# Optimization experiments

Measured on AMD Instinct MI355X. Metric: run time of the kernel, lower is better.

Reference implementation:

```python
import jax, jax.numpy as jnp
import numpy as np

N_NODES = 100000
N_EDGES = 1600000
D_IN = 128
D_HID = 128


def setup_inputs() -> dict:
    key = jax.random.key(0)
    k1, k2, k3, k4 = jax.random.split(key, 4)
    x = jax.random.normal(k1, (N_NODES, D_IN), dtype=jnp.float32)
    edge_index = jax.random.randint(k2, (2, N_EDGES), 0, N_NODES, dtype=jnp.int32)
    # glorot-style init for the two GCNConv linear weights
    s1 = (6.0 / (D_IN + D_HID)) ** 0.5
    s2 = (6.0 / (D_HID + D_HID)) ** 0.5
    W1 = jax.random.uniform(k3, (D_IN, D_HID), dtype=jnp.float32, minval=-s1, maxval=s1)
    W2 = jax.random.uniform(k4, (D_HID, D_HID), dtype=jnp.float32, minval=-s2, maxval=s2)
    b1 = jnp.zeros((D_HID,), dtype=jnp.float32)
    b2 = jnp.zeros((D_HID,), dtype=jnp.float32)
    return {"x": x, "edge_index": edge_index, "W1": W1, "b1": b1, "W2": W2, "b2": b2}


def _gcn_conv(h, src, dst, norm, W, b, num_nodes):
    # PyG GCNConv: linear transform, then normalized scatter-add aggregation, then bias.
    h = h @ W                                   # [N, D]
    msg = h[src] * norm[:, None]                # [E+N, D] gathered + scaled messages
    agg = jax.ops.segment_sum(msg, dst, num_segments=num_nodes)
    return agg + b


def reference(x, edge_index, W1, b1, W2, b2):
    n = x.shape[0]
    loops = jnp.arange(n, dtype=edge_index.dtype)
    src = jnp.concatenate([edge_index[0], loops])  # add self-loops
    dst = jnp.concatenate([edge_index[1], loops])
    # symmetric normalization D^{-1/2} (A+I) D^{-1/2}, degree computed on targets
    deg = jax.ops.segment_sum(jnp.ones_like(dst, dtype=x.dtype), dst, num_segments=n)
    dinv = jnp.where(deg > 0, jax.lax.rsqrt(jnp.maximum(deg, 1.0)), 0.0)
    norm = dinv[src] * dinv[dst]
    h = jax.nn.relu(_gcn_conv(x, src, dst, norm, W1, b1, n))
    h = jax.nn.relu(_gcn_conv(h, src, dst, norm, W2, b2, n))
    return h
```

## Files before the change

### kernel.cpp

```cpp
#include <hip/hip_runtime.h>

#define D 128
#define BSH 8
#define BNODES (1 << BSH)
#define NCHUNK 512
#define MAXB 512

typedef __attribute__((ext_vector_type(8))) __bf16 bf16x8;
typedef __attribute__((ext_vector_type(4))) float f32x4;

__device__ __forceinline__ unsigned short f2bf(float f) {
    unsigned int u = __float_as_uint(f);
    u += 0x7fffu + ((u >> 16) & 1u);
    return (unsigned short)(u >> 16);
}
__device__ __forceinline__ float lo_f(unsigned u) { return __uint_as_float(u << 16); }
__device__ __forceinline__ float hi_f(unsigned u) { return __uint_as_float(u & 0xffff0000u); }


__global__ __launch_bounds__(256) void k_hist(const int* __restrict__ dst,
                                              int* __restrict__ cnts,
                                              int E, int nbkt, int chunk) {
    __shared__ int hist[MAXB];
    int c = blockIdx.x;
    int t = threadIdx.x;
    for (int i = t; i < nbkt; i += 256) hist[i] = 0;
    __syncthreads();
    int e0 = c * chunk, e1 = min(e0 + chunk, E);
    for (int e = e0 + t; e < e1; e += 256) atomicAdd(&hist[dst[e] >> BSH], 1);
    __syncthreads();
    for (int i = t; i < nbkt; i += 256) cnts[(size_t)i * NCHUNK + c] = hist[i];
}

__global__ __launch_bounds__(256) void k_chunksum(int* __restrict__ cnts,
                                                  int* __restrict__ btot, int nbkt) {
    int b = blockIdx.x * 4 + (threadIdx.x >> 6);
    if (b >= nbkt) return;
    int l = threadIdx.x & 63;
    int carry = 0;
    for (int g = 0; g < NCHUNK; g += 64) {
        int v = cnts[(size_t)b * NCHUNK + g + l];
        int x = v;
#pragma unroll
        for (int off = 1; off < 64; off <<= 1) {
            int u = __shfl_up(x, off);
            if (l >= off) x += u;
        }
        cnts[(size_t)b * NCHUNK + g + l] = carry + x - v;
        carry += __shfl(x, 63);
    }
    if (l == 0) btot[b] = carry;
}

__global__ __launch_bounds__(MAXB) void k_bktscan(const int* __restrict__ btot,
                                                  int* __restrict__ bbase, int nbkt) {
    __shared__ int s[MAXB];
    int t = threadIdx.x;
    int v = (t < nbkt) ? btot[t] : 0;
    s[t] = v;
    __syncthreads();
    for (int off = 1; off < MAXB; off <<= 1) {
        int u = (t >= off) ? s[t - off] : 0;
        __syncthreads();
        s[t] += u;
        __syncthreads();
    }
    if (t < nbkt) bbase[t + 1] = s[t];
    if (t == 0) bbase[0] = 0;
}

__global__ __launch_bounds__(256) void k_place(const int* __restrict__ src,
                                               const int* __restrict__ dst,
                                               const int* __restrict__ cnts,
                                               const int* __restrict__ bbase,
                                               unsigned* __restrict__ pairs,
                                               int E, int nbkt, int chunk) {
    __shared__ int cur[MAXB];
    int c = blockIdx.x;
    int t = threadIdx.x;
    for (int i = t; i < nbkt; i += 256)
        cur[i] = bbase[i] + cnts[(size_t)i * NCHUNK + c];
    __syncthreads();
    int e0 = c * chunk, e1 = min(e0 + chunk, E);
    for (int e = e0 + t; e < e1; e += 256) {
        int d = dst[e];
        int p = atomicAdd(&cur[d >> BSH], 1);
        pairs[p] = ((unsigned)(d & (BNODES - 1)) << 24) | (unsigned)src[e];
    }
}

__global__ __launch_bounds__(BNODES) void k_build(const unsigned* __restrict__ pairs,
                                                  const int* __restrict__ bbase,
                                                  int* __restrict__ rp,
                                                  float* __restrict__ dinv,
                                                  int* __restrict__ col, int N) {
    __shared__ int cntL[BNODES];
    __shared__ int lcur[BNODES];
    int b = blockIdx.x;
    int n0 = b << BSH;
    int t = threadIdx.x;
    int e0 = bbase[b], e1 = bbase[b + 1];

    cntL[t] = 0;
    __syncthreads();
    for (int e = e0 + t; e < e1; e += BNODES)
        atomicAdd(&cntL[pairs[e] >> 24], 1);
    __syncthreads();
    int deg = cntL[t];
    for (int off = 1; off < BNODES; off <<= 1) {
        int u = (t >= off) ? cntL[t - off] : 0;
        __syncthreads();
        cntL[t] += u;
        __syncthreads();
    }
    int rpv = e0 + cntL[t] - deg;
    lcur[t] = rpv;
    int node = n0 + t;
    if (node < N) {
        rp[node] = rpv;
        dinv[node] = rsqrtf((float)deg + 1.0f);
        if (node == N - 1) rp[N] = e1;
    }
    __syncthreads();
    for (int e = e0 + t; e < e1; e += BNODES) {
        unsigned v = pairs[e];
        int p = atomicAdd(&lcur[v >> 24], 1);
        col[p] = (int)(v & 0x00FFFFFFu);
    }
}

__global__ __launch_bounds__(256) void k_cvt(const float* __restrict__ x,
                                             const float* __restrict__ dinv,
                                             unsigned short* __restrict__ y, int nchunk) {
    int g = blockIdx.x * blockDim.x + threadIdx.x;
    if (g >= nchunk) return;
    int row = g >> 5;
    float s = dinv[row];
    float4 v = reinterpret_cast<const float4*>(x)[g];
    ushort4 o;
    o.x = f2bf(v.x * s);
    o.y = f2bf(v.y * s);
    o.z = f2bf(v.z * s);
    o.w = f2bf(v.w * s);
    reinterpret_cast<ushort4*>(y)[g] = o;
}

__global__ __launch_bounds__(256) void k_agg(const unsigned short* __restrict__ y,
                                             unsigned* __restrict__ outp,
                                             const int* __restrict__ col,
                                             const int* __restrict__ rp,
                                             const float* __restrict__ dinv, int n) {
    int node = blockIdx.x * 4 + (threadIdx.x >> 6);
    if (node >= n) return;
    int c = threadIdx.x & 63;
    const unsigned* yv = reinterpret_cast<const unsigned*>(y);

    unsigned v = yv[(size_t)node * 64 + c];
    float a0 = lo_f(v), a1 = hi_f(v);

    int e0 = rp[node], e1 = rp[node + 1];
    int e = e0;
    for (; e + 8 <= e1; e += 8) {
        int s[8];
#pragma unroll
        for (int i = 0; i < 8; ++i) s[i] = col[e + i];
        unsigned u[8];
#pragma unroll
        for (int i = 0; i < 8; ++i) u[i] = yv[(size_t)s[i] * 64 + c];
#pragma unroll
        for (int i = 0; i < 8; ++i) { a0 += lo_f(u[i]); a1 += hi_f(u[i]); }
    }
    for (; e + 4 <= e1; e += 4) {
        int s0 = col[e], s1 = col[e + 1], s2 = col[e + 2], s3 = col[e + 3];
        unsigned u0 = yv[(size_t)s0 * 64 + c];
        unsigned u1 = yv[(size_t)s1 * 64 + c];
        unsigned u2 = yv[(size_t)s2 * 64 + c];
        unsigned u3 = yv[(size_t)s3 * 64 + c];
        a0 += (lo_f(u0) + lo_f(u1)) + (lo_f(u2) + lo_f(u3));
        a1 += (hi_f(u0) + hi_f(u1)) + (hi_f(u2) + hi_f(u3));
    }
    for (; e < e1; ++e) {
        unsigned u = yv[(size_t)col[e] * 64 + c];
        a0 += lo_f(u);
        a1 += hi_f(u);
    }
    float dn = dinv[node];
    unsigned o = ((unsigned)f2bf(a1 * dn) << 16) | (unsigned)f2bf(a0 * dn);
    outp[(size_t)node * 64 + c] = o;
}

template <int STORE_BF16>
__global__ __launch_bounds__(256) void k_mfma(const unsigned short* __restrict__ A,
                                              const float* __restrict__ W,
                                              const float* __restrict__ bias,
                                              float* __restrict__ out_f32,
                                              unsigned short* __restrict__ out_bf16,
                                              const float* __restrict__ dinv, int N) {
    __shared__ unsigned short Wt[128][136];
    int tid = threadIdx.x;
#pragma unroll
    for (int i = 0; i < 64; ++i) {
        int idx = tid + i * 256;
        int k = idx >> 7, c = idx & 127;
        Wt[c][k] = f2bf(W[idx]);
    }
    __syncthreads();

    int wv = tid >> 6, l = tid & 63;
    int lr = l & 15, lg = l >> 4;
    int r0 = blockIdx.x * 128 + wv * 32;

    f32x4 acc[2][8];
#pragma unroll
    for (int mi = 0; mi < 2; ++mi)
#pragma unroll
        for (int nf = 0; nf < 8; ++nf) acc[mi][nf] = (f32x4)(0.0f);

#pragma unroll
    for (int k0 = 0; k0 < 128; k0 += 32) {
        bf16x8 a[2];
#pragma unroll
        for (int mi = 0; mi < 2; ++mi) {
            int r = r0 + mi * 16 + lr;
            if (r >= N) r = N - 1;
            a[mi] = *reinterpret_cast<const bf16x8*>(&A[(size_t)r * 128 + k0 + lg * 8]);
        }
#pragma unroll
        for (int nf = 0; nf < 8; ++nf) {
            bf16x8 b = *reinterpret_cast<const bf16x8*>(&Wt[nf * 16 + lr][k0 + lg * 8]);
            acc[0][nf] = __builtin_amdgcn_mfma_f32_16x16x32_bf16(a[0], b, acc[0][nf], 0, 0, 0);
            acc[1][nf] = __builtin_amdgcn_mfma_f32_16x16x32_bf16(a[1], b, acc[1][nf], 0, 0, 0);
        }
    }

    float bv[8];
#pragma unroll
    for (int nf = 0; nf < 8; ++nf) bv[nf] = bias[nf * 16 + lr];

#pragma unroll
    for (int mi = 0; mi < 2; ++mi) {
#pragma unroll
        for (int q = 0; q < 4; ++q) {
            int r = r0 + mi * 16 + lg * 4 + q;
            if (r < N) {
                float dv = 1.0f;
                if (STORE_BF16) dv = dinv[r];
#pragma unroll
                for (int nf = 0; nf < 8; ++nf) {
                    int ccol = nf * 16 + lr;
                    float vv = fmaxf(acc[mi][nf][q] + bv[nf], 0.0f);
                    if (STORE_BF16)
                        out_bf16[(size_t)r * 128 + ccol] = f2bf(vv * dv);
                    else
                        out_f32[(size_t)r * 128 + ccol] = vv;
                }
            }
        }
    }
}


extern "C" void kernel_launch(void* const* d_in, const int* in_sizes, int n_in,
                              void* d_out, int out_size, void* d_ws, size_t ws_size,
                              hipStream_t stream) {
    const float* x  = (const float*)d_in[0];
    const int*   ei = (const int*)d_in[1];
    const float* W1 = (const float*)d_in[2];
    const float* b1 = (const float*)d_in[3];
    const float* W2 = (const float*)d_in[4];
    const float* b2 = (const float*)d_in[5];
    float* out = (float*)d_out;

    const int N = in_sizes[0] / D;
    const int E = in_sizes[1] / 2;
    const int* src = ei;
    const int* dst = ei + E;
    const int NBKT = (N + BNODES - 1) >> BSH;
    const int CHUNK = (E + NCHUNK - 1) / NCHUNK;

    char* w = (char*)d_ws;
    auto alloc = [&](size_t bytes) -> void* {
        void* p = (void*)w;
        w += (bytes + 255) & ~(size_t)255;
        return p;
    };
    float* dinv     = (float*)alloc((size_t)N * 4);
    int* rp         = (int*)alloc((size_t)(N + 1) * 4);
    int* cnts       = (int*)alloc((size_t)NBKT * NCHUNK * 4);
    int* btot       = (int*)alloc((size_t)NBKT * 4);
    int* bbase      = (int*)alloc((size_t)(NBKT + 1) * 4);
    unsigned* pairs = (unsigned*)alloc((size_t)E * 4);
    int* col        = (int*)alloc((size_t)E * 4);
    unsigned short* y    = (unsigned short*)alloc((size_t)N * D * 2);
    unsigned short* Abuf = (unsigned short*)alloc((size_t)N * D * 2);

    k_hist<<<NCHUNK, 256, 0, stream>>>(dst, cnts, E, NBKT, CHUNK);
    k_chunksum<<<(NBKT + 3) / 4, 256, 0, stream>>>(cnts, btot, NBKT);
    k_bktscan<<<1, MAXB, 0, stream>>>(btot, bbase, NBKT);
    k_place<<<NCHUNK, 256, 0, stream>>>(src, dst, cnts, bbase, pairs, E, NBKT, CHUNK);
    k_build<<<NBKT, BNODES, 0, stream>>>(pairs, bbase, rp, dinv, col, N);

    const int nchunk = N * (D / 4);
    const int aggblocks = (N + 3) / 4;
    const int gemmblocks = (N + 127) / 128;

    k_cvt<<<(nchunk + 255) / 256, 256, 0, stream>>>(x, dinv, y, nchunk);
    k_agg<<<aggblocks, 256, 0, stream>>>(y, (unsigned*)Abuf, col, rp, dinv, N);
    k_mfma<1><<<gemmblocks, 256, 0, stream>>>(Abuf, W1, b1, nullptr, y, dinv, N);
    k_agg<<<aggblocks, 256, 0, stream>>>(y, (unsigned*)Abuf, col, rp, dinv, N);
    k_mfma<0><<<gemmblocks, 256, 0, stream>>>(Abuf, W2, b2, out, nullptr, dinv, N);
}
```

Measured before the change: 239.3 us.

## Fuse neighbor aggregation with MFMA GEMM and pre-transpose weights once

Merges the gather-aggregate kernel and the MFMA GEMM into one kernel per layer. Each block aggregates 64 nodes into a shared-memory bf16 tile, then multiplies it by a pre-converted transposed weight matrix read from global memory. This removes the intermediate Abuf write/read and two launches, and drops the per-block weight conversion into LDS. In exchange, each wave aggregates 16 nodes serially before the GEMM, the GEMM tile is smaller, and the weight B-fragments come from global/L2 rather than LDS.

```diff
diff --git a/kernel.cpp b/kernel.cpp
--- a/kernel.cpp
+++ b/kernel.cpp
@@ -145,92 +145,87 @@
     reinterpret_cast<ushort4*>(y)[g] = o;
 }
 
-__global__ __launch_bounds__(256) void k_agg(const unsigned short* __restrict__ y,
-                                             unsigned* __restrict__ outp,
-                                             const int* __restrict__ col,
-                                             const int* __restrict__ rp,
-                                             const float* __restrict__ dinv, int n) {
-    int node = blockIdx.x * 4 + (threadIdx.x >> 6);
-    if (node >= n) return;
-    int c = threadIdx.x & 63;
+__global__ __launch_bounds__(256) void k_wcvt(const float* __restrict__ W1,
+                                              const float* __restrict__ W2,
+                                              unsigned short* __restrict__ Wt1,
+                                              unsigned short* __restrict__ Wt2) {
+    int idx = blockIdx.x * 256 + threadIdx.x;
+    const float* W = (idx < 16384) ? W1 : W2;
+    unsigned short* Wt = (idx < 16384) ? Wt1 : Wt2;
+    int i = idx & 16383;
+    int c = i >> 7, k = i & 127;
+    Wt[(size_t)c * 128 + k] = f2bf(W[(size_t)k * 128 + c]);
+}
+
+template <int STORE_BF16>
+__global__ __launch_bounds__(256) void k_aggmm(const unsigned short* __restrict__ y,
+                                               const unsigned short* __restrict__ Wt,
+                                               const float* __restrict__ bias,
+                                               const int* __restrict__ col,
+                                               const int* __restrict__ rp,
+                                               const float* __restrict__ dinv,
+                                               float* __restrict__ out_f32,
+                                               unsigned short* __restrict__ out_bf16,
+                                               int N) {
+    __shared__ unsigned As[64][68];
+    int tid = threadIdx.x;
+    int wv = tid >> 6, l = tid & 63;
+    int r0 = blockIdx.x * 64;
     const unsigned* yv = reinterpret_cast<const unsigned*>(y);
 
-    unsigned v = yv[(size_t)node * 64 + c];
-    float a0 = lo_f(v), a1 = hi_f(v);
-
-    int e0 = rp[node], e1 = rp[node + 1];
-    int e = e0;
-    for (; e + 8 <= e1; e += 8) {
-        int s[8];
-#pragma unroll
-        for (int i = 0; i < 8; ++i) s[i] = col[e + i];
-        unsigned u[8];
-#pragma unroll
-        for (int i = 0; i < 8; ++i) u[i] = yv[(size_t)s[i] * 64 + c];
-#pragma unroll
-        for (int i = 0; i < 8; ++i) { a0 += lo_f(u[i]); a1 += hi_f(u[i]); }
-    }
-    for (; e + 4 <= e1; e += 4) {
-        int s0 = col[e], s1 = col[e + 1], s2 = col[e + 2], s3 = col[e + 3];
-        unsigned u0 = yv[(size_t)s0 * 64 + c];
-        unsigned u1 = yv[(size_t)s1 * 64 + c];
-        unsigned u2 = yv[(size_t)s2 * 64 + c];
-        unsigned u3 = yv[(size_t)s3 * 64 + c];
-        a0 += (lo_f(u0) + lo_f(u1)) + (lo_f(u2) + lo_f(u3));
-        a1 += (hi_f(u0) + hi_f(u1)) + (hi_f(u2) + hi_f(u3));
-    }
-    for (; e < e1; ++e) {
-        unsigned u = yv[(size_t)col[e] * 64 + c];
-        a0 += lo_f(u);
-        a1 += hi_f(u);
-    }
-    float dn = dinv[node];
-    unsigned o = ((unsigned)f2bf(a1 * dn) << 16) | (unsigned)f2bf(a0 * dn);
-    outp[(size_t)node * 64 + c] = o;
-}
-
-template <int STORE_BF16>
-__global__ __launch_bounds__(256) void k_mfma(const unsigned short* __restrict__ A,
-                                              const float* __restrict__ W,
-                                              const float* __restrict__ bias,
-                                              float* __restrict__ out_f32,
-                                              unsigned short* __restrict__ out_bf16,
-                                              const float* __restrict__ dinv, int N) {
-    __shared__ unsigned short Wt[128][136];
-    int tid = threadIdx.x;
-#pragma unroll
-    for (int i = 0; i < 64; ++i) {
-        int idx = tid + i * 256;
-        int k = idx >> 7, c = idx & 127;
-        Wt[c][k] = f2bf(W[idx]);
-    }
-    __syncthreads();
-
-    int wv = tid >> 6, l = tid & 63;
+    for (int i = 0; i < 16; ++i) {
+        int node = r0 + wv * 16 + i;
+        unsigned o = 0u;
+        if (node < N) {
+            unsigned v = yv[(size_t)node * 64 + l];
+            float a0 = lo_f(v), a1 = hi_f(v);
+            int e0 = rp[node], e1 = rp[node + 1];
+            int e = e0;
+            for (; e + 8 <= e1; e += 8) {
+                int s[8];
+#pragma unroll
+                for (int j = 0; j < 8; ++j) s[j] = col[e + j];
+                unsigned u[8];
+#pragma unroll
+                for (int j = 0; j < 8; ++j) u[j] = yv[(size_t)s[j] * 64 + l];
+#pragma unroll
+                for (int j = 0; j < 8; ++j) { a0 += lo_f(u[j]); a1 += hi_f(u[j]); }
+            }
+            for (; e + 4 <= e1; e += 4) {
+                int s0 = col[e], s1 = col[e + 1], s2 = col[e + 2], s3 = col[e + 3];
+                unsigned u0 = yv[(size_t)s0 * 64 + l];
+                unsigned u1 = yv[(size_t)s1 * 64 + l];
+                unsigned u2 = yv[(size_t)s2 * 64 + l];
+                unsigned u3 = yv[(size_t)s3 * 64 + l];
+                a0 += (lo_f(u0) + lo_f(u1)) + (lo_f(u2) + lo_f(u3));
+                a1 += (hi_f(u0) + hi_f(u1)) + (hi_f(u2) + hi_f(u3));
+            }
+            for (; e < e1; ++e) {
+                unsigned u = yv[(size_t)col[e] * 64 + l];
+                a0 += lo_f(u);
+                a1 += hi_f(u);
+            }
+            float dn = dinv[node];
+            o = ((unsigned)f2bf(a1 * dn) << 16) | (unsigned)f2bf(a0 * dn);
+        }
+        As[wv * 16 + i][l] = o;
+    }
+    __syncthreads();
+
     int lr = l & 15, lg = l >> 4;
-    int r0 = blockIdx.x * 128 + wv * 32;
-
-    f32x4 acc[2][8];
-#pragma unroll
-    for (int mi = 0; mi < 2; ++mi)
-#pragma unroll
-        for (int nf = 0; nf < 8; ++nf) acc[mi][nf] = (f32x4)(0.0f);
+    f32x4 acc[8];
+#pragma unroll
+    for (int nf = 0; nf < 8; ++nf) acc[nf] = (f32x4)(0.0f);
 
 #pragma unroll
     for (int k0 = 0; k0 < 128; k0 += 32) {
-        bf16x8 a[2];
-#pragma unroll
-        for (int mi = 0; mi < 2; ++mi) {
-            int r = r0 + mi * 16 + lr;
-            if (r >= N) r = N - 1;
-            a[mi] = *reinterpret_cast<const bf16x8*>(&A[(size_t)r * 128 + k0 + lg * 8]);
+        bf16x8 a = *reinterpret_cast<const bf16x8*>(&As[wv * 16 + lr][(k0 >> 1) + lg * 4]);
+#pragma unroll
+        for (int nf = 0; nf < 8; ++nf) {
+            bf16x8 b = *reinterpret_cast<const bf16x8*>(
+                &Wt[(size_t)(nf * 16 + lr) * 128 + k0 + lg * 8]);
+            acc[nf] = __builtin_amdgcn_mfma_f32_16x16x32_bf16(a, b, acc[nf], 0, 0, 0);
         }
-#pragma unroll
-        for (int nf = 0; nf < 8; ++nf) {
-            bf16x8 b = *reinterpret_cast<const bf16x8*>(&Wt[nf * 16 + lr][k0 + lg * 8]);
-            acc[0][nf] = __builtin_amdgcn_mfma_f32_16x16x32_bf16(a[0], b, acc[0][nf], 0, 0, 0);
-            acc[1][nf] = __builtin_amdgcn_mfma_f32_16x16x32_bf16(a[1], b, acc[1][nf], 0, 0, 0);
-        }
     }
 
     float bv[8];
@@ -238,22 +233,19 @@
     for (int nf = 0; nf < 8; ++nf) bv[nf] = bias[nf * 16 + lr];
 
 #pragma unroll
-    for (int mi = 0; mi < 2; ++mi) {
-#pragma unroll
-        for (int q = 0; q < 4; ++q) {
-            int r = r0 + mi * 16 + lg * 4 + q;
-            if (r < N) {
-                float dv = 1.0f;
-                if (STORE_BF16) dv = dinv[r];
-#pragma unroll
-                for (int nf = 0; nf < 8; ++nf) {
-                    int ccol = nf * 16 + lr;
-                    float vv = fmaxf(acc[mi][nf][q] + bv[nf], 0.0f);
-                    if (STORE_BF16)
-                        out_bf16[(size_t)r * 128 + ccol] = f2bf(vv * dv);
-                    else
-                        out_f32[(size_t)r * 128 + ccol] = vv;
-                }
+    for (int q = 0; q < 4; ++q) {
+        int r = r0 + wv * 16 + lg * 4 + q;
+        if (r < N) {
+            float dv = 1.0f;
+            if (STORE_BF16) dv = dinv[r];
+#pragma unroll
+            for (int nf = 0; nf < 8; ++nf) {
+                int ccol = nf * 16 + lr;
+                float vv = fmaxf(acc[nf][q] + bv[nf], 0.0f);
+                if (STORE_BF16)
+                    out_bf16[(size_t)r * 128 + ccol] = f2bf(vv * dv);
+                else
+                    out_f32[(size_t)r * 128 + ccol] = vv;
             }
         }
     }
@@ -291,22 +283,24 @@
     int* bbase      = (int*)alloc((size_t)(NBKT + 1) * 4);
     unsigned* pairs = (unsigned*)alloc((size_t)E * 4);
     int* col        = (int*)alloc((size_t)E * 4);
-    unsigned short* y    = (unsigned short*)alloc((size_t)N * D * 2);
-    unsigned short* Abuf = (unsigned short*)alloc((size_t)N * D * 2);
+    unsigned short* y   = (unsigned short*)alloc((size_t)N * D * 2);
+    unsigned short* y2  = (unsigned short*)alloc((size_t)N * D * 2);
+    unsigned short* Wt1 = (unsigned short*)alloc((size_t)D * D * 2);
+    unsigned short* Wt2 = (unsigned short*)alloc((size_t)D * D * 2);
 
     k_hist<<<NCHUNK, 256, 0, stream>>>(dst, cnts, E, NBKT, CHUNK);
     k_chunksum<<<(NBKT + 3) / 4, 256, 0, stream>>>(cnts, btot, NBKT);
     k_bktscan<<<1, MAXB, 0, stream>>>(btot, bbase, NBKT);
     k_place<<<NCHUNK, 256, 0, stream>>>(src, dst, cnts, bbase, pairs, E, NBKT, CHUNK);
     k_build<<<NBKT, BNODES, 0, stream>>>(pairs, bbase, rp, dinv, col, N);
+    k_wcvt<<<128, 256, 0, stream>>>(W1, W2, Wt1, Wt2);
 
     const int nchunk = N * (D / 4);
-    const int aggblocks = (N + 3) / 4;
-    const int gemmblocks = (N + 127) / 128;
+    const int fusedblocks = (N + 63) / 64;
 
     k_cvt<<<(nchunk + 255) / 256, 256, 0, stream>>>(x, dinv, y, nchunk);
-    k_agg<<<aggblocks, 256, 0, stream>>>(y, (unsigned*)Abuf, col, rp, dinv, N);
-    k_mfma<1><<<gemmblocks, 256, 0, stream>>>(Abuf, W1, b1, nullptr, y, dinv, N);
-    k_agg<<<aggblocks, 256, 0, stream>>>(y, (unsigned*)Abuf, col, rp, dinv, N);
-    k_mfma<0><<<gemmblocks, 256, 0, stream>>>(Abuf, W2, b2, out, nullptr, dinv, N);
-}
+    k_aggmm<1><<<fusedblocks, 256, 0, stream>>>(y, Wt1, b1, col, rp, dinv,
+                                                nullptr, y2, N);
+    k_aggmm<0><<<fusedblocks, 256, 0, stream>>>(y2, Wt2, b2, col, rp, dinv,
+                                                out, nullptr, N);
+}
```

Measured after the change: 321.2 us. 1.34x slower.

## Slice features into 16-column panels for cache-friendly gather aggregation

Applied to the files above, without the earlier changes.

Stores the bf16 feature matrices panel-major: 8 panels of 16 columns, each panel holding all nodes contiguously. The aggregation runs one pass per panel, so a 3.2MB panel can stay cached across random neighbor gathers. Each wave covers 8 edges at a time with 8 lanes per row, then reduces across lanes with shuffles. The weight transpose and bf16 conversion move into a separate one-time kernel, so the GEMM reads pre-transposed weights from global memory instead of rebuilding them in LDS per block. In exchange, each gather moves only 32 bytes per row, the aggregation launches 8x more blocks, and the GEMM and conversion kernels need strided panel indexing.

```diff
diff --git a/kernel.cpp b/kernel.cpp
--- a/kernel.cpp
+++ b/kernel.cpp
@@ -131,81 +131,97 @@
 
 __global__ __launch_bounds__(256) void k_cvt(const float* __restrict__ x,
                                              const float* __restrict__ dinv,
-                                             unsigned short* __restrict__ y, int nchunk) {
-    int g = blockIdx.x * blockDim.x + threadIdx.x;
-    if (g >= nchunk) return;
-    int row = g >> 5;
-    float s = dinv[row];
-    float4 v = reinterpret_cast<const float4*>(x)[g];
-    ushort4 o;
-    o.x = f2bf(v.x * s);
-    o.y = f2bf(v.y * s);
-    o.z = f2bf(v.z * s);
-    o.w = f2bf(v.w * s);
-    reinterpret_cast<ushort4*>(y)[g] = o;
-}
-
-__global__ __launch_bounds__(256) void k_agg(const unsigned short* __restrict__ y,
-                                             unsigned* __restrict__ outp,
-                                             const int* __restrict__ col,
-                                             const int* __restrict__ rp,
-                                             const float* __restrict__ dinv, int n) {
-    int node = blockIdx.x * 4 + (threadIdx.x >> 6);
-    if (node >= n) return;
-    int c = threadIdx.x & 63;
-    const unsigned* yv = reinterpret_cast<const unsigned*>(y);
-
-    unsigned v = yv[(size_t)node * 64 + c];
-    float a0 = lo_f(v), a1 = hi_f(v);
-
+                                             unsigned short* __restrict__ ys, int N) {
+    __shared__ unsigned As[64][65];
+    int t = threadIdx.x;
+    int n0 = blockIdx.x * 64;
+#pragma unroll
+    for (int i = 0; i < 8; ++i) {
+        int idx = i * 256 + t;
+        int r = idx >> 5;
+        int c4 = idx & 31;
+        if (n0 + r < N) {
+            float4 v = reinterpret_cast<const float4*>(x)[(size_t)(n0 + r) * 32 + c4];
+            float s = dinv[n0 + r];
+            As[r][c4 * 2]     = ((unsigned)f2bf(v.y * s) << 16) | (unsigned)f2bf(v.x * s);
+            As[r][c4 * 2 + 1] = ((unsigned)f2bf(v.w * s) << 16) | (unsigned)f2bf(v.z * s);
+        }
+    }
+    __syncthreads();
+    int r = t >> 2, j = t & 3;
+    if (n0 + r < N) {
+#pragma unroll
+        for (int p = 0; p < 8; ++p) {
+            uint2 w2 = make_uint2(As[r][p * 8 + 2 * j], As[r][p * 8 + 2 * j + 1]);
+            reinterpret_cast<uint2*>(ys)[((size_t)p * N + n0 + r) * 4 + j] = w2;
+        }
+    }
+}
+
+__global__ __launch_bounds__(256) void k_wcvt(const float* __restrict__ W1,
+                                              const float* __restrict__ W2,
+                                              unsigned short* __restrict__ Wt1,
+                                              unsigned short* __restrict__ Wt2) {
+    int idx = blockIdx.x * 256 + threadIdx.x;
+    const float* W = (idx < 16384) ? W1 : W2;
+    unsigned short* Wt = (idx < 16384) ? Wt1 : Wt2;
+    int i = idx & 16383;
+    int c = i >> 7, k = i & 127;
+    Wt[(size_t)c * 128 + k] = f2bf(W[(size_t)k * 128 + c]);
+}
+
+__global__ __launch_bounds__(256) void k_aggs(const unsigned* __restrict__ ys,
+                                              unsigned* __restrict__ os,
+                                              const int* __restrict__ col,
+                                              const int* __restrict__ rp,
+                                              const float* __restrict__ dinv,
+                                              int N, int nblk) {
+    int pass = blockIdx.x / nblk;
+    int node = (blockIdx.x - pass * nblk) * 4 + (threadIdx.x >> 6);
+    if (node >= N) return;
+    int l = threadIdx.x & 63;
+    int g = l >> 3;
+    int f = l & 7;
+    const unsigned* base = ys + (size_t)pass * N * 8;
+
+    float a0 = 0.0f, a1 = 0.0f;
     int e0 = rp[node], e1 = rp[node + 1];
-    int e = e0;
-    for (; e + 8 <= e1; e += 8) {
-        int s[8];
-#pragma unroll
-        for (int i = 0; i < 8; ++i) s[i] = col[e + i];
-        unsigned u[8];
-#pragma unroll
-        for (int i = 0; i < 8; ++i) u[i] = yv[(size_t)s[i] * 64 + c];
-#pragma unroll
-        for (int i = 0; i < 8; ++i) { a0 += lo_f(u[i]); a1 += hi_f(u[i]); }
-    }
-    for (; e + 4 <= e1; e += 4) {
-        int s0 = col[e], s1 = col[e + 1], s2 = col[e + 2], s3 = col[e + 3];
-        unsigned u0 = yv[(size_t)s0 * 64 + c];
-        unsigned u1 = yv[(size_t)s1 * 64 + c];
-        unsigned u2 = yv[(size_t)s2 * 64 + c];
-        unsigned u3 = yv[(size_t)s3 * 64 + c];
-        a0 += (lo_f(u0) + lo_f(u1)) + (lo_f(u2) + lo_f(u3));
-        a1 += (hi_f(u0) + hi_f(u1)) + (hi_f(u2) + hi_f(u3));
-    }
-    for (; e < e1; ++e) {
-        unsigned u = yv[(size_t)col[e] * 64 + c];
+    int e = e0 + g;
+    for (; e + 8 < e1; e += 16) {
+        int s0 = col[e], s1 = col[e + 8];
+        unsigned u0 = base[(size_t)s0 * 8 + f];
+        unsigned u1 = base[(size_t)s1 * 8 + f];
+        a0 += lo_f(u0) + lo_f(u1);
+        a1 += hi_f(u0) + hi_f(u1);
+    }
+    if (e < e1) {
+        unsigned u = base[(size_t)col[e] * 8 + f];
         a0 += lo_f(u);
         a1 += hi_f(u);
     }
-    float dn = dinv[node];
-    unsigned o = ((unsigned)f2bf(a1 * dn) << 16) | (unsigned)f2bf(a0 * dn);
-    outp[(size_t)node * 64 + c] = o;
+#pragma unroll
+    for (int m = 8; m < 64; m <<= 1) {
+        a0 += __shfl_xor(a0, m);
+        a1 += __shfl_xor(a1, m);
+    }
+    if (g == 0) {
+        unsigned v = base[(size_t)node * 8 + f];
+        a0 += lo_f(v);
+        a1 += hi_f(v);
+        float dn = dinv[node];
+        os[(size_t)pass * N * 8 + (size_t)node * 8 + f] =
+            ((unsigned)f2bf(a1 * dn) << 16) | (unsigned)f2bf(a0 * dn);
+    }
 }
 
 template <int STORE_BF16>
 __global__ __launch_bounds__(256) void k_mfma(const unsigned short* __restrict__ A,
-                                              const float* __restrict__ W,
+                                              const unsigned short* __restrict__ Wt,
                                               const float* __restrict__ bias,
                                               float* __restrict__ out_f32,
                                               unsigned short* __restrict__ out_bf16,
                                               const float* __restrict__ dinv, int N) {
-    __shared__ unsigned short Wt[128][136];
     int tid = threadIdx.x;
-#pragma unroll
-    for (int i = 0; i < 64; ++i) {
-        int idx = tid + i * 256;
-        int k = idx >> 7, c = idx & 127;
-        Wt[c][k] = f2bf(W[idx]);
-    }
-    __syncthreads();
-
     int wv = tid >> 6, l = tid & 63;
     int lr = l & 15, lg = l >> 4;
     int r0 = blockIdx.x * 128 + wv * 32;
@@ -218,16 +234,19 @@
 
 #pragma unroll
     for (int k0 = 0; k0 < 128; k0 += 32) {
+        int p = (k0 >> 4) + (lg >> 1);
+        int hoff = (lg & 1) * 8;
         bf16x8 a[2];
 #pragma unroll
         for (int mi = 0; mi < 2; ++mi) {
             int r = r0 + mi * 16 + lr;
             if (r >= N) r = N - 1;
-            a[mi] = *reinterpret_cast<const bf16x8*>(&A[(size_t)r * 128 + k0 + lg * 8]);
+            a[mi] = *reinterpret_cast<const bf16x8*>(&A[((size_t)p * N + r) * 16 + hoff]);
         }
 #pragma unroll
         for (int nf = 0; nf < 8; ++nf) {
-            bf16x8 b = *reinterpret_cast<const bf16x8*>(&Wt[nf * 16 + lr][k0 + lg * 8]);
+            bf16x8 b = *reinterpret_cast<const bf16x8*>(
+                &Wt[(size_t)(nf * 16 + lr) * 128 + k0 + lg * 8]);
             acc[0][nf] = __builtin_amdgcn_mfma_f32_16x16x32_bf16(a[0], b, acc[0][nf], 0, 0, 0);
             acc[1][nf] = __builtin_amdgcn_mfma_f32_16x16x32_bf16(a[1], b, acc[1][nf], 0, 0, 0);
         }
@@ -247,12 +266,11 @@
                 if (STORE_BF16) dv = dinv[r];
 #pragma unroll
                 for (int nf = 0; nf < 8; ++nf) {
-                    int ccol = nf * 16 + lr;
                     float vv = fmaxf(acc[mi][nf][q] + bv[nf], 0.0f);
                     if (STORE_BF16)
-                        out_bf16[(size_t)r * 128 + ccol] = f2bf(vv * dv);
+                        out_bf16[((size_t)nf * N + r) * 16 + lr] = f2bf(vv * dv);
                     else
-                        out_f32[(size_t)r * 128 + ccol] = vv;
+                        out_f32[(size_t)r * 128 + nf * 16 + lr] = vv;
                 }
             }
         }
@@ -291,22 +309,28 @@
     int* bbase      = (int*)alloc((size_t)(NBKT + 1) * 4);
     unsigned* pairs = (unsigned*)alloc((size_t)E * 4);
     int* col        = (int*)alloc((size_t)E * 4);
-    unsigned short* y    = (unsigned short*)alloc((size_t)N * D * 2);
-    unsigned short* Abuf = (unsigned short*)alloc((size_t)N * D * 2);
+    unsigned short* ys  = (unsigned short*)alloc((size_t)N * D * 2);
+    unsigned short* as_ = (unsigned short*)alloc((size_t)N * D * 2);
+    unsigned short* y2s = (unsigned short*)alloc((size_t)N * D * 2);
+    unsigned short* Wt1 = (unsigned short*)alloc((size_t)D * D * 2);
+    unsigned short* Wt2 = (unsigned short*)alloc((size_t)D * D * 2);
 
     k_hist<<<NCHUNK, 256, 0, stream>>>(dst, cnts, E, NBKT, CHUNK);
     k_chunksum<<<(NBKT + 3) / 4, 256, 0, stream>>>(cnts, btot, NBKT);
     k_bktscan<<<1, MAXB, 0, stream>>>(btot, bbase, NBKT);
     k_place<<<NCHUNK, 256, 0, stream>>>(src, dst, cnts, bbase, pairs, E, NBKT, CHUNK);
     k_build<<<NBKT, BNODES, 0, stream>>>(pairs, bbase, rp, dinv, col, N);
-
-    const int nchunk = N * (D / 4);
-    const int aggblocks = (N + 3) / 4;
+    k_wcvt<<<128, 256, 0, stream>>>(W1, W2, Wt1, Wt2);
+
+    const int nblk = (N + 3) / 4;
+    const int cvtblocks = (N + 63) / 64;
     const int gemmblocks = (N + 127) / 128;
 
-    k_cvt<<<(nchunk + 255) / 256, 256, 0, stream>>>(x, dinv, y, nchunk);
-    k_agg<<<aggblocks, 256, 0, stream>>>(y, (unsigned*)Abuf, col, rp, dinv, N);
-    k_mfma<1><<<gemmblocks, 256, 0, stream>>>(Abuf, W1, b1, nullptr, y, dinv, N);
-    k_agg<<<aggblocks, 256, 0, stream>>>(y, (unsigned*)Abuf, col, rp, dinv, N);
-    k_mfma<0><<<gemmblocks, 256, 0, stream>>>(Abuf, W2, b2, out, nullptr, dinv, N);
-}
+    k_cvt<<<cvtblocks, 256, 0, stream>>>(x, dinv, ys, N);
+    k_aggs<<<nblk * 8, 256, 0, stream>>>((const unsigned*)ys, (unsigned*)as_,
+                                         col, rp, dinv, N, nblk);
+    k_mfma<1><<<gemmblocks, 256, 0, stream>>>(as_, Wt1, b1, nullptr, y2s, dinv, N);
+    k_aggs<<<nblk * 8, 256, 0, stream>>>((const unsigned*)y2s, (unsigned*)as_,
+                                         col, rp, dinv, N, nblk);
+    k_mfma<0><<<gemmblocks, 256, 0, stream>>>(as_, Wt2, b2, out, nullptr, dinv, N);
+}
```

New measurement: 583.6 us. 144% more time.
